# Kernel tuning notes

Measured on AMD Instinct MI355X. Metric: run time of the kernel, lower is better.

## Reference

```python
import jax, jax.numpy as jnp
import numpy as np

B, N, K, C = 8, 4096, 2048, 256


def setup_inputs() -> dict:
    key = jax.random.key(0)
    kx, ka, kp = jax.random.split(key, 3)
    x = jax.random.normal(kx, (B, K, C), dtype=jnp.float32)
    A = jax.random.uniform(ka, (B, N, N), dtype=jnp.float32)
    # idx mask with EXACTLY K ones per batch row (TopKPool keeps a fixed count)
    perms = jax.vmap(lambda k: jax.random.permutation(k, N))(jax.random.split(kp, B))
    idx = jnp.zeros((B, N), dtype=jnp.int32).at[jnp.arange(B)[:, None], perms[:, :K]].set(1)
    return {"x": x, "idx": idx, "A": A}


def reference(x, idx, A):
    # x: [B, K, C] pooled features; idx: [B, N] 0/1 selection mask; A: [B, N, N] (only N is used)
    b, k, c = x.shape
    n = A.shape[1]
    mask = idx > 0
    # Stable argsort puts the (exactly k) selected positions first, in increasing node order,
    # matching tf.where's ordering of nonzero indices.
    order = jnp.argsort(jnp.where(mask, 0, 1), axis=1, stable=True)  # [B, N]
    sel = order[:, :k]  # [B, K] node positions to receive the pooled features
    out = jnp.zeros((b, n, c), dtype=x.dtype)
    out = out.at[jnp.arange(b)[:, None], sel].set(x)  # single batched parallel scatter
    return out
```

## Files before the change

### kernel.cpp

```cpp
#include <hip/hip_runtime.h>

#define BB 8
#define NN 4096
#define KK 2048
#define C4 64

__global__ __launch_bounds__(256) void topk_fused_kernel(const float4* __restrict__ x,
                                                         const int* __restrict__ idx,
                                                         float4* __restrict__ out) {
    const int bi = blockIdx.x;
    const int b = bi >> 8;
    const int rowStart = (bi & 255) << 4;
    const int t = threadIdx.x;
    const int lane = t & 63;
    const int wave = t >> 6;

    const int4* idxB4 = (const int4*)(idx + (size_t)b * NN);

    const int4 v4 = idxB4[(rowStart >> 2) + wave];
    const long long outRow0 = (long long)b * NN + rowStart + wave * 4;
    const float4 z = make_float4(0.f, 0.f, 0.f, 0.f);
    if (v4.x <= 0) out[(outRow0 + 0) * C4 + lane] = z;
    if (v4.y <= 0) out[(outRow0 + 1) * C4 + lane] = z;
    if (v4.z <= 0) out[(outRow0 + 2) * C4 + lane] = z;
    if (v4.w <= 0) out[(outRow0 + 3) * C4 + lane] = z;

    __shared__ int waveSum[4];
    __shared__ int waveLoc[4];

    int partial = 0;
    const int n4 = rowStart >> 2;
#pragma unroll
    for (int i = 0; i < 4; ++i) {
        const int j = t + i * 256;
        if (j < n4) {
            const int4 v = idxB4[j];
            partial += v.x + v.y + v.z + v.w;
        }
    }
#pragma unroll
    for (int off = 32; off > 0; off >>= 1)
        partial += __shfl_down(partial, off, 64);
    if (lane == 0) {
        waveSum[wave] = partial;
        waveLoc[wave] = v4.x + v4.y + v4.z + v4.w;
    }
    __syncthreads();

    const int4 s = *(const int4*)waveSum;
    int preW = 0;
    for (int w = 0; w < wave; ++w) preW += waveLoc[w];
    const long long r0 = (long long)b * KK + (s.x + s.y + s.z + s.w) + preW;

    const long long r1 = r0 + (v4.x > 0 ? 1 : 0);
    const long long r2 = r1 + (v4.y > 0 ? 1 : 0);
    const long long r3 = r2 + (v4.z > 0 ? 1 : 0);

    float4 val0, val1, val2, val3;
    if (v4.x > 0) val0 = x[r0 * C4 + lane];
    if (v4.y > 0) val1 = x[r1 * C4 + lane];
    if (v4.z > 0) val2 = x[r2 * C4 + lane];
    if (v4.w > 0) val3 = x[r3 * C4 + lane];

    if (v4.x > 0) out[(outRow0 + 0) * C4 + lane] = val0;
    if (v4.y > 0) out[(outRow0 + 1) * C4 + lane] = val1;
    if (v4.z > 0) out[(outRow0 + 2) * C4 + lane] = val2;
    if (v4.w > 0) out[(outRow0 + 3) * C4 + lane] = val3;
}

extern "C" void kernel_launch(void* const* d_in, const int* in_sizes, int n_in,
                              void* d_out, int out_size, void* d_ws, size_t ws_size,
                              hipStream_t stream) {
    const float* x  = (const float*)d_in[0];
    const int* idx  = (const int*)d_in[1];
    float* out = (float*)d_out;

    topk_fused_kernel<<<(BB * NN) / 16, 256, 0, stream>>>(
        (const float4*)x, idx, (float4*)out);
}
```

Before: 13.53 us.

## Compute per-wave prefix independently using suffix sums to drop block sync

Each wave now computes its own exclusive prefix count. Waves in the first half sum the mask entries before them, and waves in the second half sum the entries after them and subtract from K, so no wave reads more than half the row. This removes the shared-memory exchange and the __syncthreads, and uses an xor-shuffle allreduce within each wave. The price is redundant mask reads, since every wave rescans its own range. Correctness relies on each batch row having exactly K selected entries, which the task guarantees. Index arithmetic also moves from 64-bit to 32-bit.

```diff
diff --git a/kernel.cpp b/kernel.cpp
--- a/kernel.cpp
+++ b/kernel.cpp
@@ -10,51 +10,44 @@
                                                          float4* __restrict__ out) {
     const int bi = blockIdx.x;
     const int b = bi >> 8;
-    const int rowStart = (bi & 255) << 4;
-    const int t = threadIdx.x;
-    const int lane = t & 63;
-    const int wave = t >> 6;
+    const int wave = threadIdx.x >> 6;
+    const int lane = threadIdx.x & 63;
+    const int row4 = ((bi & 255) << 2) + wave;
 
-    const int4* idxB4 = (const int4*)(idx + (size_t)b * NN);
+    const int4* idxB4 = (const int4*)(idx + b * NN);
 
-    const int4 v4 = idxB4[(rowStart >> 2) + wave];
-    const long long outRow0 = (long long)b * NN + rowStart + wave * 4;
+    const int4 v4 = idxB4[row4];
+
+    const bool front = (row4 <= 512);
+    const int i0 = front ? lane : (row4 + lane);
+    const int lim = front ? row4 : 1024;
+    int s = 0;
+#pragma unroll
+    for (int k = 0; k < 8; ++k) {
+        const int i = i0 + (k << 6);
+        if (i < lim) {
+            const int4 v = idxB4[i];
+            s += v.x + v.y + v.z + v.w;
+        }
+    }
+
+    const int outRow0 = (b << 12) + (row4 << 2);
     const float4 z = make_float4(0.f, 0.f, 0.f, 0.f);
     if (v4.x <= 0) out[(outRow0 + 0) * C4 + lane] = z;
     if (v4.y <= 0) out[(outRow0 + 1) * C4 + lane] = z;
     if (v4.z <= 0) out[(outRow0 + 2) * C4 + lane] = z;
     if (v4.w <= 0) out[(outRow0 + 3) * C4 + lane] = z;
 
-    __shared__ int waveSum[4];
-    __shared__ int waveLoc[4];
+#pragma unroll
+    for (int off = 1; off < 64; off <<= 1)
+        s += __shfl_xor(s, off, 64);
 
-    int partial = 0;
-    const int n4 = rowStart >> 2;
-#pragma unroll
-    for (int i = 0; i < 4; ++i) {
-        const int j = t + i * 256;
-        if (j < n4) {
-            const int4 v = idxB4[j];
-            partial += v.x + v.y + v.z + v.w;
-        }
-    }
-#pragma unroll
-    for (int off = 32; off > 0; off >>= 1)
-        partial += __shfl_down(partial, off, 64);
-    if (lane == 0) {
-        waveSum[wave] = partial;
-        waveLoc[wave] = v4.x + v4.y + v4.z + v4.w;
-    }
-    __syncthreads();
+    const int base = front ? s : (KK - s);
 
-    const int4 s = *(const int4*)waveSum;
-    int preW = 0;
-    for (int w = 0; w < wave; ++w) preW += waveLoc[w];
-    const long long r0 = (long long)b * KK + (s.x + s.y + s.z + s.w) + preW;
-
-    const long long r1 = r0 + (v4.x > 0 ? 1 : 0);
-    const long long r2 = r1 + (v4.y > 0 ? 1 : 0);
-    const long long r3 = r2 + (v4.z > 0 ? 1 : 0);
+    const int r0 = (b << 11) + base;
+    const int r1 = r0 + (v4.x > 0 ? 1 : 0);
+    const int r2 = r1 + (v4.y > 0 ? 1 : 0);
+    const int r3 = r2 + (v4.z > 0 ? 1 : 0);
 
     float4 val0, val1, val2, val3;
     if (v4.x > 0) val0 = x[r0 * C4 + lane];
```

Result: slower. 14.03 us (+3.7%).
